# Kernel tuning notes

Measured on AMD Instinct MI355X. Metric: run time of the kernel, lower is better.

Reference implementation:

```python
import jax, jax.numpy as jnp
import numpy as np

COMMITMENT_COST = 0.25
N_EMBED = 1024
EMB_DIM = 256

def setup_inputs() -> dict:
    key = jax.random.key(0)
    k1, k2 = jax.random.split(key)
    z = jax.random.normal(k1, (32, EMB_DIM, 32, 32), dtype=jnp.float32)
    # embedding.weight.data.uniform_(-1/n_embed, 1/n_embed)
    embedding = jax.random.uniform(k2, (N_EMBED, EMB_DIM), dtype=jnp.float32,
                                   minval=-1.0 / N_EMBED, maxval=1.0 / N_EMBED)
    return {"z": z, "embedding": embedding}

def reference(z, embedding):
    # NCHW -> NHWC
    zp = jnp.transpose(z, (0, 2, 3, 1))            # [B,H,W,D]
    in_shape = zp.shape
    flat = zp.reshape(-1, in_shape[-1])            # [N,D]
    # squared L2 distances (argmin equivalent to p=2 cdist argmin)
    d2 = (jnp.sum(flat * flat, axis=1, keepdims=True)
          - 2.0 * (flat @ embedding.T)
          + jnp.sum(embedding * embedding, axis=1))  # [N,K]
    idx = jnp.argmin(d2, axis=1)                   # [N]
    # one-hot @ codebook == direct gather
    z_quant = embedding[idx].reshape(in_shape)     # [B,H,W,D]
    codebook_loss = jnp.mean((z_quant - jax.lax.stop_gradient(zp)) ** 2)
    commitment_loss = jnp.mean((zp - jax.lax.stop_gradient(z_quant)) ** 2)
    loss = codebook_loss + COMMITMENT_COST * commitment_loss
    # straight-through estimator
    z_st = zp + jax.lax.stop_gradient(z_quant - zp)
    z_st = jnp.transpose(z_st, (0, 3, 1, 2))       # NHWC -> NCHW
    return (z_st, loss, codebook_loss, commitment_loss)
```

## Files before the change

kernel.cpp:

```cpp
#include <hip/hip_runtime.h>
#include <hip/hip_bf16.h>
#include <stdint.h>


typedef short v8s __attribute__((ext_vector_type(8)));
typedef float v4f __attribute__((ext_vector_type(4)));

__device__ inline unsigned short f2bf(float f) {
    uint32_t u = __float_as_uint(f);
    return (unsigned short)((u + 0x7fffu + ((u >> 16) & 1u)) >> 16);
}

__global__ __launch_bounds__(512) void k_prep_a(const float* __restrict__ z,
                                                unsigned short* __restrict__ Abf) {
    int tid = threadIdx.x;
    int b = blockIdx.x >> 4, hw0 = (blockIdx.x & 15) << 6;
    int t15 = tid & 15, dblk = tid >> 4;
    const float* zp = z + ((size_t)b << 18) + (size_t)(dblk << 3) * 1024 + hw0 + (t15 << 2);
    float4 L[8];
#pragma unroll
    for (int j = 0; j < 8; j++)
        L[j] = *(const float4*)(zp + (size_t)j * 1024);
    const float* Lf = (const float*)L;
    v8s* Aout = (v8s*)Abf + ((size_t)(b * 1024 + hw0 + (t15 << 2))) * 32 + dblk;
#pragma unroll
    for (int c = 0; c < 4; c++) {
        union { v8s v; unsigned short s[8]; } u;
#pragma unroll
        for (int j = 0; j < 8; j++) u.s[j] = f2bf(Lf[j * 4 + c]);
        Aout[(size_t)c * 32] = u.v;
    }
}

__global__ __launch_bounds__(256) void k_prep_e(const float* __restrict__ E,
                                                v8s* __restrict__ Esw,
                                                float* __restrict__ nE,
                                                float* __restrict__ accum) {
    __shared__ float Ef[16][264];
    int q = blockIdx.x, tid = threadIdx.x;
    const float4* Ein = (const float4*)(E + ((size_t)q << 12));
#pragma unroll
    for (int i = 0; i < 4; i++) {
        int f4 = i * 256 + tid;
        int row = f4 >> 6, c4 = (f4 & 63) << 2;
        *(float4*)&Ef[row][c4] = Ein[f4];
    }
    __syncthreads();
    {
        int c = tid >> 4, l = tid & 15;
        float s = 0.f;
#pragma unroll
        for (int j = 0; j < 16; j++) { float v = Ef[c][l + 16 * j]; s += v * v; }
#pragma unroll
        for (int off = 1; off < 16; off <<= 1) s += __shfl_xor(s, off);
        if (l == 0) nE[q * 16 + c] = 0.5f * s;
    }
#pragma unroll
    for (int i = 0; i < 2; i++) {
        int u = tid + i * 256;
        int um = u & 15, ug = (u >> 4) & 3, udc = (u >> 6) & 7;
        int d0 = udc * 32 + ug * 8;
        union { v8s v; unsigned short s[8]; } pk;
#pragma unroll
        for (int e = 0; e < 8; e++) pk.s[e] = f2bf(Ef[um][d0 + e]);
        Esw[((size_t)q << 9) + u] = pk.v;
    }
    if (q == 0 && tid == 0) accum[0] = 0.f;
}

__global__ __launch_bounds__(512) void k_main(
        const unsigned short* __restrict__ Abf,
        const v8s* __restrict__ Esw,
        const float* __restrict__ nE,
        const float* __restrict__ z,
        const float* __restrict__ E,
        float* __restrict__ out,
        float* __restrict__ accum) {
    __shared__ union {
        v8s    B[2][2048];
        float4 Eg4[2048];
    } S;
    __shared__ float nEl[1024];
    __shared__ int   idxLds[128];
    __shared__ float w8[8];

    int tid = threadIdx.x;
    int lane = tid & 63, w = tid >> 6;
    int g = lane >> 4, m = lane & 15;
    int R0 = blockIdx.x << 7;
    int b = R0 >> 10;

#pragma unroll
    for (int i = 0; i < 2; i++) nEl[tid + i * 512] = nE[tid + i * 512];

    v8s a[8];
    {
        const v8s* Ap = (const v8s*)Abf;
        int row = R0 + w * 16 + m;
#pragma unroll
        for (int dc = 0; dc < 8; dc++)
            a[dc] = Ap[(size_t)row * 32 + dc * 4 + g];
    }

#define STAGE(ch, buf)                                                        \
    {                                                                         \
        _Pragma("unroll")                                                     \
        for (int j = 0; j < 4; j++) {                                         \
            __builtin_amdgcn_global_load_lds(                                 \
                (const __attribute__((address_space(1))) void*)               \
                    (Esw + ((size_t)(ch) << 11) + (j << 9) + (w << 6) + lane),\
                (__attribute__((address_space(3))) void*)                     \
                    &S.B[buf][(j << 9) + (w << 6)],                           \
                16, 0, 0);                                                    \
        }                                                                     \
    }

    float best[4]; int bidx[4];
#pragma unroll
    for (int r = 0; r < 4; r++) { best[r] = 3.4e38f; bidx[r] = 0; }

    STAGE(0, 0);
#pragma unroll 1
    for (int ct = 0; ct < 16; ct++) {
        int cur = ct & 1;
        __syncthreads();
        if (ct < 15) STAGE(ct + 1, cur ^ 1);
        float ne[4];
#pragma unroll
        for (int t = 0; t < 4; t++) ne[t] = nEl[(ct << 6) + t * 16 + m];
        v4f acc[4];
#pragma unroll
        for (int t = 0; t < 4; t++) acc[t] = (v4f){0.f, 0.f, 0.f, 0.f};
#pragma unroll
        for (int dc = 0; dc < 8; dc++) {
#pragma unroll
            for (int t = 0; t < 4; t++) {
                v8s bf = S.B[cur][t * 512 + dc * 64 + g * 16 + m];
                acc[t] = __builtin_amdgcn_mfma_f32_16x16x32_bf16(a[dc], bf, acc[t], 0, 0, 0);
            }
        }
#pragma unroll
        for (int t = 0; t < 4; t++) {
            int code = (ct << 6) + t * 16 + m;
#pragma unroll
            for (int r = 0; r < 4; r++) {
                float s0 = ne[t] - acc[t][r];
                if (s0 < best[r]) { best[r] = s0; bidx[r] = code; }
            }
        }
    }

#pragma unroll
    for (int r = 0; r < 4; r++) {
        uint32_t sb = __float_as_uint(best[r]);
        sb = (sb & 0x80000000u) ? ~sb : (sb | 0x80000000u);
        unsigned long long pk = ((unsigned long long)sb << 32) | (uint32_t)bidx[r];
#pragma unroll
        for (int off = 1; off < 16; off <<= 1) {
            unsigned long long o = __shfl_xor(pk, off);
            if (o < pk) pk = o;
        }
        if (m == 0)
            idxLds[w * 16 + g * 4 + r] = (int)(pk & 0xffffffffu);
    }
    __syncthreads();

    float lsum = 0.f;
    const float* zb = z + ((size_t)b << 18);
    float* ob = out + ((size_t)b << 18);
    int hwl = tid & 31, dq0 = tid >> 5;
#pragma unroll 1
    for (int ph = 0; ph < 4; ph++) {
#pragma unroll
        for (int i = 0; i < 4; i++) {
            int row = w + (i << 3);
            int k = idxLds[(ph << 5) + row];
            float4 v = ((const float4*)(E + ((size_t)k << 8)))[lane];
            S.Eg4[(row << 6) + (lane ^ row)] = v;
        }
        __syncthreads();
        int hwp = (R0 & 1023) + (ph << 5) + hwl;
#pragma unroll
        for (int i = 0; i < 4; i++) {
            int dq = dq0 + (i << 4);
            float4 ev = S.Eg4[(hwl << 6) + (dq ^ hwl)];
            size_t o = ((size_t)dq << 12) + hwp;
            float z0 = zb[o], z1 = zb[o + 1024], z2 = zb[o + 2048], z3 = zb[o + 3072];
            ob[o] = ev.x; ob[o + 1024] = ev.y; ob[o + 2048] = ev.z; ob[o + 3072] = ev.w;
            float dx = ev.x - z0, dy = ev.y - z1, dz2 = ev.z - z2, dw = ev.w - z3;
            lsum += dx * dx + dy * dy + dz2 * dz2 + dw * dw;
        }
        __syncthreads();
    }
#pragma unroll
    for (int off = 1; off < 64; off <<= 1) lsum += __shfl_xor(lsum, off);
    if (lane == 0) w8[w] = lsum;
    __syncthreads();
    if (tid == 0) {
        float s = 0.f;
#pragma unroll
        for (int i = 0; i < 8; i++) s += w8[i];
        atomicAdd(accum, s);
    }
#undef STAGE
}

__global__ void k_loss(const float* __restrict__ accum, float* __restrict__ out) {
    if (threadIdx.x == 0) {
        float s = accum[0] * (1.0f / 8388608.0f);
        out[8388608] = 1.25f * s;
        out[8388609] = s;
        out[8388610] = s;
    }
}

extern "C" void kernel_launch(void* const* d_in, const int* in_sizes, int n_in,
                              void* d_out, int out_size, void* d_ws, size_t ws_size,
                              hipStream_t stream) {
    const float* z = (const float*)d_in[0];
    const float* E = (const float*)d_in[1];
    char* ws = (char*)d_ws;
    unsigned short* Abf   = (unsigned short*)(ws);
    v8s*            Esw   = (v8s*)(ws + 16777216);
    float*          nE    = (float*)(ws + 17301504);
    float*          accum = (float*)(ws + 17305600);
    float* out = (float*)d_out;

    hipLaunchKernelGGL(k_prep_e, dim3(64),  dim3(256), 0, stream, E, Esw, nE, accum);
    hipLaunchKernelGGL(k_prep_a, dim3(512), dim3(512), 0, stream, z, Abf);
    hipLaunchKernelGGL(k_main,   dim3(256), dim3(512), 0, stream,
                       Abf, Esw, nE, z, E, out, accum);
    hipLaunchKernelGGL(k_loss,   dim3(1),   dim3(64),  0, stream, accum, out);
}
```

Before: 127.9 us.

## Fuse z bf16 conversion into main kernel and compute loss from distances

Removes the separate prep kernel that wrote a bf16 copy of z to workspace. The main kernel now loads z directly, converts it to bf16 into swizzled shared memory, and reads its A fragments from there. The per-row norm is computed from the bf16 values. The loss is then derived algebraically from the best distance plus that norm, so z no longer has to be re-read in the epilogue. This drops one kernel launch and a large global write and read round trip. In exchange the loss now uses the bf16-approximated distance rather than the exact fp32 difference, which may change accuracy.

Result: faster. 121.3 us (-5.2%).

```diff
diff --git a/kernel.cpp b/kernel.cpp
--- a/kernel.cpp
+++ b/kernel.cpp
@@ -9,27 +9,6 @@
 __device__ inline unsigned short f2bf(float f) {
     uint32_t u = __float_as_uint(f);
     return (unsigned short)((u + 0x7fffu + ((u >> 16) & 1u)) >> 16);
-}
-
-__global__ __launch_bounds__(512) void k_prep_a(const float* __restrict__ z,
-                                                unsigned short* __restrict__ Abf) {
-    int tid = threadIdx.x;
-    int b = blockIdx.x >> 4, hw0 = (blockIdx.x & 15) << 6;
-    int t15 = tid & 15, dblk = tid >> 4;
-    const float* zp = z + ((size_t)b << 18) + (size_t)(dblk << 3) * 1024 + hw0 + (t15 << 2);
-    float4 L[8];
-#pragma unroll
-    for (int j = 0; j < 8; j++)
-        L[j] = *(const float4*)(zp + (size_t)j * 1024);
-    const float* Lf = (const float*)L;
-    v8s* Aout = (v8s*)Abf + ((size_t)(b * 1024 + hw0 + (t15 << 2))) * 32 + dblk;
-#pragma unroll
-    for (int c = 0; c < 4; c++) {
-        union { v8s v; unsigned short s[8]; } u;
-#pragma unroll
-        for (int j = 0; j < 8; j++) u.s[j] = f2bf(Lf[j * 4 + c]);
-        Aout[(size_t)c * 32] = u.v;
-    }
 }
 
 __global__ __launch_bounds__(256) void k_prep_e(const float* __restrict__ E,
@@ -69,7 +48,6 @@
 }
 
 __global__ __launch_bounds__(512) void k_main(
-        const unsigned short* __restrict__ Abf,
         const v8s* __restrict__ Esw,
         const float* __restrict__ nE,
         const float* __restrict__ z,
@@ -88,19 +66,57 @@
     int lane = tid & 63, w = tid >> 6;
     int g = lane >> 4, m = lane & 15;
     int R0 = blockIdx.x << 7;
-    int b = R0 >> 10;
-
+    int b = R0 >> 10, hw0 = R0 & 1023;
+
+    {
+        int q = tid & 31, dblk = tid >> 5;
+        const float* zp = z + ((size_t)b << 18) + hw0 + (q << 2);
+#pragma unroll
+        for (int s = 0; s < 2; s++) {
+            float4 L[8];
+#pragma unroll
+            for (int j = 0; j < 8; j++)
+                L[j] = *(const float4*)(zp + (size_t)(((dblk << 4) + (s << 3) + j) << 10));
+            const float* Lf = (const float*)L;
+            int slot = (dblk << 1) + s;
+#pragma unroll
+            for (int c = 0; c < 4; c++) {
+                union { v8s v; unsigned short u[8]; } pk;
+#pragma unroll
+                for (int j = 0; j < 8; j++) pk.u[j] = f2bf(Lf[j * 4 + c]);
+                int row = (q << 2) + c;
+                int sw = slot ^ ((row ^ (row >> 2)) & 7);
+                *(v8s*)((char*)&S + (row << 9) + (sw << 4)) = pk.v;
+            }
+        }
+    }
 #pragma unroll
     for (int i = 0; i < 2; i++) nEl[tid + i * 512] = nE[tid + i * 512];
+    __syncthreads();
 
     v8s a[8];
+    float nrm = 0.f;
     {
-        const v8s* Ap = (const v8s*)Abf;
-        int row = R0 + w * 16 + m;
-#pragma unroll
-        for (int dc = 0; dc < 8; dc++)
-            a[dc] = Ap[(size_t)row * 32 + dc * 4 + g];
-    }
+        int row = (w << 4) + m;
+        int f = (row ^ (row >> 2)) & 7;
+#pragma unroll
+        for (int dc = 0; dc < 8; dc++) {
+            int sw = ((dc << 2) + g) ^ f;
+            a[dc] = *(const v8s*)((const char*)&S + (row << 9) + (sw << 4));
+        }
+#pragma unroll
+        for (int dc = 0; dc < 8; dc++) {
+            union { v8s v; unsigned short u[8]; } un; un.v = a[dc];
+#pragma unroll
+            for (int j = 0; j < 8; j++) {
+                float v = __uint_as_float((uint32_t)un.u[j] << 16);
+                nrm = fmaf(v, v, nrm);
+            }
+        }
+        nrm += __shfl_xor(nrm, 16);
+        nrm += __shfl_xor(nrm, 32);
+    }
+    __syncthreads();
 
 #define STAGE(ch, buf)                                                        \
     {                                                                         \
@@ -150,6 +166,7 @@
         }
     }
 
+    float lsum = 0.f;
 #pragma unroll
     for (int r = 0; r < 4; r++) {
         uint32_t sb = __float_as_uint(best[r]);
@@ -160,13 +177,16 @@
             unsigned long long o = __shfl_xor(pk, off);
             if (o < pk) pk = o;
         }
-        if (m == 0)
+        float rn = __shfl(nrm, (g << 2) + r);
+        if (m == 0) {
             idxLds[w * 16 + g * 4 + r] = (int)(pk & 0xffffffffu);
-    }
-    __syncthreads();
-
-    float lsum = 0.f;
-    const float* zb = z + ((size_t)b << 18);
+            uint32_t t = (uint32_t)(pk >> 32);
+            float sw = __uint_as_float((t & 0x80000000u) ? (t & 0x7fffffffu) : ~t);
+            lsum += 2.0f * sw + rn;
+        }
+    }
+    __syncthreads();
+
     float* ob = out + ((size_t)b << 18);
     int hwl = tid & 31, dq0 = tid >> 5;
 #pragma unroll 1
@@ -179,16 +199,13 @@
             S.Eg4[(row << 6) + (lane ^ row)] = v;
         }
         __syncthreads();
-        int hwp = (R0 & 1023) + (ph << 5) + hwl;
+        int hwp = hw0 + (ph << 5) + hwl;
 #pragma unroll
         for (int i = 0; i < 4; i++) {
             int dq = dq0 + (i << 4);
             float4 ev = S.Eg4[(hwl << 6) + (dq ^ hwl)];
             size_t o = ((size_t)dq << 12) + hwp;
-            float z0 = zb[o], z1 = zb[o + 1024], z2 = zb[o + 2048], z3 = zb[o + 3072];
             ob[o] = ev.x; ob[o + 1024] = ev.y; ob[o + 2048] = ev.z; ob[o + 3072] = ev.w;
-            float dx = ev.x - z0, dy = ev.y - z1, dz2 = ev.z - z2, dw = ev.w - z3;
-            lsum += dx * dx + dy * dy + dz2 * dz2 + dw * dw;
         }
         __syncthreads();
     }
@@ -220,15 +237,13 @@
     const float* z = (const float*)d_in[0];
     const float* E = (const float*)d_in[1];
     char* ws = (char*)d_ws;
-    unsigned short* Abf   = (unsigned short*)(ws);
-    v8s*            Esw   = (v8s*)(ws + 16777216);
-    float*          nE    = (float*)(ws + 17301504);
-    float*          accum = (float*)(ws + 17305600);
+    v8s*   Esw   = (v8s*)(ws);
+    float* nE    = (float*)(ws + 524288);
+    float* accum = (float*)(ws + 528384);
     float* out = (float*)d_out;
 
     hipLaunchKernelGGL(k_prep_e, dim3(64),  dim3(256), 0, stream, E, Esw, nE, accum);
-    hipLaunchKernelGGL(k_prep_a, dim3(512), dim3(512), 0, stream, z, Abf);
     hipLaunchKernelGGL(k_main,   dim3(256), dim3(512), 0, stream,
-                       Abf, Esw, nE, z, E, out, accum);
+                       Esw, nE, z, E, out, accum);
     hipLaunchKernelGGL(k_loss,   dim3(1),   dim3(64),  0, stream, accum, out);
 }
```
